# Optimization experiments

Hardware: AMD Instinct MI355X
Metric: run time of the kernel (lower is better)

The kernel has to match this reference:

```python
import jax, jax.numpy as jnp
import numpy as np

DIM = 768
HEADS = 12
MLP_DIM = 3072
EPS = 1e-5


def setup_inputs() -> dict:
    key = jax.random.key(0)
    ks = jax.random.split(key, 10)
    s = lambda d: 1.0 / np.sqrt(d)
    return {
        "x": jax.random.normal(ks[0], (8, 1024, DIM), dtype=jnp.float32),
        "ln1_g": jnp.ones((DIM,), jnp.float32),
        "ln1_b": jnp.zeros((DIM,), jnp.float32),
        "w_qkv": jax.random.normal(ks[1], (DIM, 3 * DIM), jnp.float32) * s(DIM),
        "w_out": jax.random.normal(ks[2], (DIM, DIM), jnp.float32) * s(DIM),
        "b_out": jnp.zeros((DIM,), jnp.float32),
        "ln2_g": jnp.ones((DIM,), jnp.float32),
        "ln2_b": jnp.zeros((DIM,), jnp.float32),
        "w1": jax.random.normal(ks[3], (DIM, MLP_DIM), jnp.float32) * s(DIM),
        "b1": jnp.zeros((MLP_DIM,), jnp.float32),
        "w2": jax.random.normal(ks[4], (MLP_DIM, DIM), jnp.float32) * s(MLP_DIM),
        "b2": jnp.zeros((DIM,), jnp.float32),
    }


def _layernorm(x, g, b):
    mu = jnp.mean(x, axis=-1, keepdims=True)
    var = jnp.mean(jnp.square(x - mu), axis=-1, keepdims=True)
    return (x - mu) * jax.lax.rsqrt(var + EPS) * g + b


def _block(x, ln1_g, ln1_b, w_qkv, w_out, b_out, ln2_g, ln2_b, w1, b1, w2, b2):
    B, N, C = x.shape
    H = HEADS
    Dh = C // H
    scale = Dh ** -0.5
    # attention
    h = _layernorm(x, ln1_g, ln1_b)
    qkv = (h @ w_qkv).reshape(B, N, 3, H, Dh)
    q, k, v = qkv[:, :, 0], qkv[:, :, 1], qkv[:, :, 2]  # [B,N,H,Dh]
    attn = jnp.einsum("bnhd,bmhd->bhnm", q, k) * scale
    attn = jax.nn.softmax(attn, axis=-1)
    o = jnp.einsum("bhnm,bmhd->bnhd", attn, v).reshape(B, N, C)
    x = x + o @ w_out + b_out
    # mlp (exact erf GELU, matching torch nn.GELU default)
    h = _layernorm(x, ln2_g, ln2_b)
    h = jax.nn.gelu(h @ w1 + b1, approximate=False)
    x = x + h @ w2 + b2
    return x


def reference(x, ln1_g, ln1_b, w_qkv, w_out, b_out, ln2_g, ln2_b, w1, b1, w2, b2):
    return _block(x, ln1_g, ln1_b, w_qkv, w_out, b_out, ln2_g, ln2_b, w1, b1, w2, b2)
```

## Files before the change

kernel.cpp:

```cpp
#include <hip/hip_runtime.h>
#include <hip/hip_bf16.h>
#include <cstdint>

#define DIM 768
#define HEADS 12
#define DH 64
#define MLP_DIM 3072
#define ROWS 8192
#define SEQ 1024
#define PPAD 72
#define ISTR 136
#define FSTR 132

typedef __attribute__((ext_vector_type(8))) short bf16x8;
typedef __attribute__((ext_vector_type(4))) float f32x4;

typedef __attribute__((address_space(1))) void GV;
typedef __attribute__((address_space(3))) void SV;

__device__ inline void async16(const void* g, void* l) {
  __builtin_amdgcn_global_load_lds((GV*)(void*)g, (SV*)l, 16, 0, 0);
}

__device__ inline unsigned short f2b(float f) {
  union { float f; uint32_t u; } v; v.f = f;
  uint32_t u = v.u;
  return (unsigned short)((u + 0x7fffu + ((u >> 16) & 1u)) >> 16);
}

__device__ inline float gelu_f(float v) {
  float x = v * 0.70710678118654752f;
  float ax = fabsf(x);
  float t = 1.f / (1.f + 0.47047f * ax);
  float poly = t * (0.3480242f + t * (-0.0958798f + t * 0.7478556f));
  float erfv = 1.f - poly * __expf(-ax * ax);
  erfv = copysignf(erfv, x);
  return 0.5f * v * (1.f + erfv);
}

__global__ __launch_bounds__(256) void transpose_k(const float* __restrict__ in,
                                                   unsigned short* __restrict__ out,
                                                   int K, int N) {
  __shared__ float t[32][33];
  int tx = threadIdx.x & 31, ty = threadIdx.x >> 5;
  int bn = blockIdx.x * 32, bk = blockIdx.y * 32;
#pragma unroll
  for (int i = ty; i < 32; i += 8) t[i][tx] = in[(size_t)(bk + i) * N + bn + tx];
  __syncthreads();
#pragma unroll
  for (int i = ty; i < 32; i += 8) out[(size_t)(bn + i) * K + bk + tx] = f2b(t[tx][i]);
}

__global__ __launch_bounds__(256) void ln_k(const float* __restrict__ x,
                                            const float* __restrict__ g,
                                            const float* __restrict__ b,
                                            unsigned short* __restrict__ h) {
  int wave = threadIdx.x >> 6, lane = threadIdx.x & 63;
  int row = blockIdx.x * 4 + wave;
  const float* xr = x + (size_t)row * DIM;
  float v[12];
  float s = 0.f;
#pragma unroll
  for (int j = 0; j < 12; ++j) { v[j] = xr[lane + j * 64]; s += v[j]; }
#pragma unroll
  for (int m = 1; m < 64; m <<= 1) s += __shfl_xor(s, m);
  float mu = s * (1.f / DIM);
  float vs = 0.f;
#pragma unroll
  for (int j = 0; j < 12; ++j) { float d = v[j] - mu; vs += d * d; }
#pragma unroll
  for (int m = 1; m < 64; m <<= 1) vs += __shfl_xor(vs, m);
  float rstd = rsqrtf(vs * (1.f / DIM) + 1e-5f);
  unsigned short* hr = h + (size_t)row * DIM;
#pragma unroll
  for (int j = 0; j < 12; ++j) {
    int i = lane + j * 64;
    hr[i] = f2b((v[j] - mu) * rstd * g[i] + b[i]);
  }
}

template <int MODE, int TM>
__global__ __launch_bounds__(256, 2) void gemm_k(
    const unsigned short* __restrict__ A, const unsigned short* __restrict__ Bt,
    int M, int N, int K,
    const float* __restrict__ bias, const float* __restrict__ resid,
    float* __restrict__ outf, unsigned short* __restrict__ outb,
    unsigned short* __restrict__ Qb, unsigned short* __restrict__ Kb,
    unsigned short* __restrict__ Vt) {
  constexpr int MI = (TM == 128) ? 4 : 2;
  constexpr int ASZ = TM * 64, BSZ = 128 * 64;
  __shared__ __align__(16) unsigned short smem[2 * (ASZ + BSZ)];
  int tid = threadIdx.x;
  int wave = tid >> 6, lane = tid & 63, lrow = lane & 15, qd = lane >> 4;
  int ntn = N >> 7;
  int bm = (blockIdx.x / ntn) * TM;
  int bn = (blockIdx.x % ntn) << 7;
  int wm = (TM == 128) ? (wave >> 1) * 64 : (wave & 1) * 32;
  int wn = (TM == 128) ? (wave & 1) * 64 : (wave >> 1) * 64;

  f32x4 acc[MI][4];
#pragma unroll
  for (int i = 0; i < MI; ++i)
#pragma unroll
    for (int j = 0; j < 4; ++j) acc[i][j] = (f32x4){0.f, 0.f, 0.f, 0.f};

  int srow = tid >> 3;
  int c = (tid & 7) ^ (srow & 7);
  const char* gA = (const char*)(A + (size_t)(bm + srow) * K) + c * 16;
  const char* gB = (const char*)(Bt + (size_t)(bn + srow) * K) + c * 16;
  size_t rstep = (size_t)32 * K * 2;

  auto stage = [&](int kt, int buf) {
    size_t ko = (size_t)kt * 128;
    char* lA = (char*)(smem + (size_t)buf * (ASZ + BSZ)) + tid * 16;
    char* lB = lA + ASZ * 2;
#pragma unroll
    for (int j = 0; j < TM / 32; ++j) async16(gA + ko + j * rstep, lA + j * 4096);
#pragma unroll
    for (int j = 0; j < 4; ++j) async16(gB + ko + j * rstep, lB + j * 4096);
  };

  int nk = K >> 6;
  stage(0, 0);
  for (int kt = 0; kt < nk; ++kt) {
    asm volatile("s_waitcnt vmcnt(0)" ::: "memory");
    __syncthreads();
    if (kt + 1 < nk) stage(kt + 1, (kt + 1) & 1);
    const unsigned short* As = smem + (size_t)(kt & 1) * (ASZ + BSZ);
    const unsigned short* Bs = As + ASZ;
#pragma unroll
    for (int s = 0; s < 2; ++s) {
      int q = s * 4 + qd;
      bf16x8 af[MI], bfr[4];
#pragma unroll
      for (int i = 0; i < MI; ++i) {
        int r = wm + i * 16 + lrow;
        af[i] = *(const bf16x8*)(As + r * 64 + ((q ^ (r & 7)) << 3));
      }
#pragma unroll
      for (int i = 0; i < 4; ++i) {
        int r = wn + i * 16 + lrow;
        bfr[i] = *(const bf16x8*)(Bs + r * 64 + ((q ^ (r & 7)) << 3));
      }
#pragma unroll
      for (int mi = 0; mi < MI; ++mi)
#pragma unroll
        for (int ni = 0; ni < 4; ++ni)
          acc[mi][ni] = __builtin_amdgcn_mfma_f32_16x16x32_bf16(af[mi], bfr[ni], acc[mi][ni], 0, 0, 0);
    }
  }
  __syncthreads();

  if (MODE == 1) {
    float* img = (float*)smem;
#pragma unroll
    for (int mi = 0; mi < MI; ++mi)
#pragma unroll
      for (int ni = 0; ni < 4; ++ni)
#pragma unroll
        for (int r = 0; r < 4; ++r)
          img[(wm + mi * 16 + qd * 4 + r) * FSTR + wn + ni * 16 + lrow] = acc[mi][ni][r];
    __syncthreads();
    int lr = tid >> 2, cs = (tid & 3) * 32;
    const float* src = img + lr * FSTR + cs;
    float* dst = outf + (size_t)(bm + lr) * 768 + bn + cs;
    const float* bp = bias + bn + cs;
    const float* rp = resid + (size_t)(bm + lr) * 768 + bn + cs;
#pragma unroll
    for (int k = 0; k < 8; ++k) {
      f32x4 v = *(const f32x4*)(src + k * 4);
      f32x4 bb = *(const f32x4*)(bp + k * 4);
      f32x4 rr = *(const f32x4*)(rp + k * 4);
      *(f32x4*)(dst + k * 4) = v + bb + rr;
    }
  } else if (MODE == 2) {
    unsigned short* img = smem;
#pragma unroll
    for (int mi = 0; mi < MI; ++mi)
#pragma unroll
      for (int ni = 0; ni < 4; ++ni)
#pragma unroll
        for (int r = 0; r < 4; ++r) {
          int lc = wn + ni * 16 + lrow;
          float v = acc[mi][ni][r] + bias[bn + lc];
          img[(wm + mi * 16 + qd * 4 + r) * ISTR + lc] = f2b(gelu_f(v));
        }
    __syncthreads();
#pragma unroll
    for (int p = 0; p < 2; ++p) {
      int lr = p * 64 + (tid >> 2);
      int cs = (tid & 3) * 32;
      const unsigned short* src = img + lr * ISTR + cs;
      unsigned short* dst = outb + (size_t)(bm + lr) * MLP_DIM + bn + cs;
#pragma unroll
      for (int k = 0; k < 4; ++k) *(uint4*)(dst + k * 8) = *(const uint4*)(src + k * 8);
    }
  } else {
    int which = bn / 768;
    int rem_base = bn - which * 768;
    unsigned short* img = smem;
    if (which < 2) {
#pragma unroll
      for (int mi = 0; mi < MI; ++mi)
#pragma unroll
        for (int ni = 0; ni < 4; ++ni)
#pragma unroll
          for (int r = 0; r < 4; ++r) {
            float v = acc[mi][ni][r];
            if (which == 0) v *= 0.125f;
            img[(wm + mi * 16 + qd * 4 + r) * ISTR + wn + ni * 16 + lrow] = f2b(v);
          }
      __syncthreads();
      int lr = tid >> 1, hseg = tid & 1;
      int hh = rem_base / 64 + hseg;
      int b = (bm + lr) >> 10, n = (bm + lr) & 1023;
      size_t bh = (size_t)(b * HEADS + hh);
      const unsigned short* src = img + lr * ISTR + hseg * 64;
      unsigned short* dst = (which == 0 ? Qb : Kb) + (bh * SEQ + n) * DH;
      if (which == 0) {
#pragma unroll
        for (int j = 0; j < 8; ++j) *(uint4*)(dst + j * 8) = *(const uint4*)(src + j * 8);
      } else {
        int nx = n & 7;
#pragma unroll
        for (int j = 0; j < 8; ++j) *(uint4*)(dst + ((j ^ nx) * 8)) = *(const uint4*)(src + j * 8);
      }
    } else {
#pragma unroll
      for (int mi = 0; mi < MI; ++mi)
#pragma unroll
        for (int ni = 0; ni < 4; ++ni) {
          int lc = wn + ni * 16 + lrow;
          int rbase = wm + mi * 16 + qd * 4;
          uint2 pk;
          pk.x = (uint32_t)f2b(acc[mi][ni][0]) | ((uint32_t)f2b(acc[mi][ni][1]) << 16);
          pk.y = (uint32_t)f2b(acc[mi][ni][2]) | ((uint32_t)f2b(acc[mi][ni][3]) << 16);
          *(uint2*)(img + lc * ISTR + rbase) = pk;
        }
      __syncthreads();
      int d = tid >> 1, nh = tid & 1;
      int hh = rem_base / 64 + (d >> 6);
      int dhl = d & 63;
      int b = bm >> 10;
      size_t bh = (size_t)(b * HEADS + hh);
      const unsigned short* src = img + d * ISTR + nh * 64;
      unsigned short* dst = Vt + (bh * DH + dhl) * SEQ + (bm & 1023) + nh * 64;
      int dx = dhl & 7;
#pragma unroll
      for (int j = 0; j < 8; ++j) *(uint4*)(dst + ((j ^ dx) * 8)) = *(const uint4*)(src + j * 8);
    }
  }
}

__global__ __launch_bounds__(256, 3) void attn_k(const unsigned short* __restrict__ Qb,
                                                 const unsigned short* __restrict__ Kb,
                                                 const unsigned short* __restrict__ Vt,
                                                 unsigned short* __restrict__ o) {
  __shared__ __align__(16) unsigned short Ks[2][64 * 64];
  __shared__ __align__(16) unsigned short Vs[2][64 * 64];
  __shared__ __align__(16) unsigned short Pa[4][32 * PPAD];
  int tid = threadIdx.x;
  int wave = tid >> 6, lane = tid & 63;
  int lrow = lane & 15, qd = lane >> 4;
  int bh = blockIdx.x % 96;
  int qt = blockIdx.x / 96;
  int b = bh / HEADS, hh = bh % HEADS;
  const unsigned short* Qh = Qb + (size_t)bh * SEQ * DH;
  const char* Kh = (const char*)(Kb + (size_t)bh * SEQ * DH);
  const char* Vh = (const char*)(Vt + (size_t)bh * DH * SEQ);
  int qw = qt * 128 + wave * 32;

  bf16x8 qf[2][2];
#pragma unroll
  for (int qs = 0; qs < 2; ++qs)
#pragma unroll
    for (int hf = 0; hf < 2; ++hf)
      qf[qs][hf] = *(const bf16x8*)(Qh + (qw + qs * 16 + lrow) * DH + hf * 32 + qd * 8);

  f32x4 oacc[2][4];
#pragma unroll
  for (int qs = 0; qs < 2; ++qs)
#pragma unroll
    for (int d = 0; d < 4; ++d) oacc[qs][d] = (f32x4){0.f, 0.f, 0.f, 0.f};
  float li[2] = {0.f, 0.f};
  unsigned short* Pw = Pa[wave];

  auto stage = [&](int t, int buf) {
    const char* kbase = Kh + (size_t)t * 8192;
    char* kd = (char*)Ks[buf];
    async16(kbase + tid * 16, kd + tid * 16);
    async16(kbase + 4096 + tid * 16, kd + 4096 + tid * 16);
    const char* vbase = Vh + (size_t)t * 128;
    char* vd = (char*)Vs[buf];
    async16(vbase + (size_t)(tid >> 3) * 2048 + (tid & 7) * 16, vd + tid * 16);
    async16(vbase + (size_t)((tid >> 3) + 32) * 2048 + (tid & 7) * 16, vd + 4096 + tid * 16);
  };

  stage(0, 0);
  for (int t = 0; t < 16; ++t) {
    asm volatile("s_waitcnt vmcnt(0)" ::: "memory");
    __syncthreads();
    if (t < 15) stage(t + 1, (t + 1) & 1);
    const unsigned short* Kst = Ks[t & 1];
    const unsigned short* Vst = Vs[t & 1];

    f32x4 st[4][2];
#pragma unroll
    for (int kt = 0; kt < 4; ++kt) {
      int krow = kt * 16 + lrow;
      int ksw = krow & 7;
      const unsigned short* Kr = Kst + krow * 64;
      bf16x8 k0 = *(const bf16x8*)(Kr + ((qd ^ ksw) << 3));
      bf16x8 k1 = *(const bf16x8*)(Kr + (((qd + 4) ^ ksw) << 3));
#pragma unroll
      for (int qs = 0; qs < 2; ++qs) {
        f32x4 z = (f32x4){0.f, 0.f, 0.f, 0.f};
        z = __builtin_amdgcn_mfma_f32_16x16x32_bf16(k0, qf[qs][0], z, 0, 0, 0);
        z = __builtin_amdgcn_mfma_f32_16x16x32_bf16(k1, qf[qs][1], z, 0, 0, 0);
        st[kt][qs] = z;
      }
    }

#pragma unroll
    for (int kt = 0; kt < 4; ++kt)
#pragma unroll
      for (int qs = 0; qs < 2; ++qs) {
        float p0 = __expf(st[kt][qs][0]);
        float p1 = __expf(st[kt][qs][1]);
        float p2 = __expf(st[kt][qs][2]);
        float p3 = __expf(st[kt][qs][3]);
        li[qs] += (p0 + p1) + (p2 + p3);
        uint2 pk;
        pk.x = (uint32_t)f2b(p0) | ((uint32_t)f2b(p1) << 16);
        pk.y = (uint32_t)f2b(p2) | ((uint32_t)f2b(p3) << 16);
        *(uint2*)(Pw + (qs * 16 + lrow) * PPAD + kt * 16 + qd * 4) = pk;
      }
    asm volatile("s_waitcnt lgkmcnt(0)" ::: "memory");

    bf16x8 ap[2][2];
#pragma unroll
    for (int qs = 0; qs < 2; ++qs)
#pragma unroll
      for (int kh = 0; kh < 2; ++kh)
        ap[qs][kh] = *(const bf16x8*)(Pw + (qs * 16 + lrow) * PPAD + kh * 32 + qd * 8);

#pragma unroll
    for (int ds = 0; ds < 4; ++ds) {
      int vrow = ds * 16 + lrow;
      int vsw = vrow & 7;
      const unsigned short* Vr = Vst + vrow * 64;
      bf16x8 v0 = *(const bf16x8*)(Vr + ((qd ^ vsw) << 3));
      bf16x8 v1 = *(const bf16x8*)(Vr + (((4 + qd) ^ vsw) << 3));
#pragma unroll
      for (int qs = 0; qs < 2; ++qs) {
        oacc[qs][ds] = __builtin_amdgcn_mfma_f32_16x16x32_bf16(ap[qs][0], v0, oacc[qs][ds], 0, 0, 0);
        oacc[qs][ds] = __builtin_amdgcn_mfma_f32_16x16x32_bf16(ap[qs][1], v1, oacc[qs][ds], 0, 0, 0);
      }
    }
  }

#pragma unroll
  for (int qs = 0; qs < 2; ++qs) {
    li[qs] += __shfl_xor(li[qs], 16);
    li[qs] += __shfl_xor(li[qs], 32);
  }

#pragma unroll
  for (int qs = 0; qs < 2; ++qs)
#pragma unroll
    for (int r = 0; r < 4; ++r) {
      float inv = 1.f / __shfl(li[qs], qd * 4 + r);
      int n = qw + qs * 16 + qd * 4 + r;
#pragma unroll
      for (int ds = 0; ds < 4; ++ds) {
        int dh = ds * 16 + lrow;
        o[((size_t)(b * SEQ + n)) * DIM + hh * DH + dh] = f2b(oacc[qs][ds][r] * inv);
      }
    }
}

extern "C" void kernel_launch(void* const* d_in, const int* in_sizes, int n_in,
                              void* d_out, int out_size, void* d_ws, size_t ws_size,
                              hipStream_t stream) {
  const float* x     = (const float*)d_in[0];
  const float* ln1_g = (const float*)d_in[1];
  const float* ln1_b = (const float*)d_in[2];
  const float* w_qkv = (const float*)d_in[3];
  const float* w_out = (const float*)d_in[4];
  const float* b_out = (const float*)d_in[5];
  const float* ln2_g = (const float*)d_in[6];
  const float* ln2_b = (const float*)d_in[7];
  const float* w1    = (const float*)d_in[8];
  const float* b1    = (const float*)d_in[9];
  const float* w2    = (const float*)d_in[10];
  const float* b2    = (const float*)d_in[11];

  char* ws = (char*)d_ws;
  unsigned short* wqkvT = (unsigned short*)(ws + 0);
  unsigned short* woutT = (unsigned short*)(ws + 3538944);
  unsigned short* w1T   = (unsigned short*)(ws + 4718592);
  unsigned short* w2T   = (unsigned short*)(ws + 9437184);
  float*          x2    = (float*)(ws + 14155776);
  unsigned short* h     = (unsigned short*)(ws + 39321600);
  char* big = ws + 51904512;
  unsigned short* Qb = (unsigned short*)(big);
  unsigned short* Kb = (unsigned short*)(big + 12582912);
  unsigned short* Vt = (unsigned short*)(big + 25165824);
  unsigned short* ob = (unsigned short*)(big + 37748736);
  unsigned short* am = (unsigned short*)(big);

  transpose_k<<<dim3(72, 24), 256, 0, stream>>>(w_qkv, wqkvT, 768, 2304);
  transpose_k<<<dim3(24, 24), 256, 0, stream>>>(w_out, woutT, 768, 768);
  transpose_k<<<dim3(96, 24), 256, 0, stream>>>(w1, w1T, 768, 3072);
  transpose_k<<<dim3(24, 96), 256, 0, stream>>>(w2, w2T, 3072, 768);

  ln_k<<<2048, 256, 0, stream>>>(x, ln1_g, ln1_b, h);
  gemm_k<0, 128><<<64 * 18, 256, 0, stream>>>(h, wqkvT, ROWS, 2304, 768,
                                              nullptr, nullptr, nullptr, nullptr, Qb, Kb, Vt);
  attn_k<<<768, 256, 0, stream>>>(Qb, Kb, Vt, ob);
  gemm_k<1, 64><<<128 * 6, 256, 0, stream>>>(ob, woutT, ROWS, 768, 768,
                                             b_out, x, x2, nullptr, nullptr, nullptr, nullptr);
  ln_k<<<2048, 256, 0, stream>>>(x2, ln2_g, ln2_b, h);
  gemm_k<2, 128><<<64 * 24, 256, 0, stream>>>(h, w1T, ROWS, 3072, 768,
                                              b1, nullptr, nullptr, am, nullptr, nullptr, nullptr);
  gemm_k<1, 64><<<128 * 6, 256, 0, stream>>>(am, w2T, ROWS, 768, 3072,
                                             b2, x2, (float*)d_out, nullptr, nullptr, nullptr, nullptr);
}
```

Measured before the change: 391.4 us.

## Split GEMM into single-buffered variants with larger per-wave tiles

Replaces the templated double-buffered GEMM with two kernels. QKV and MLP-up use 128 threads, each wave computing a 64x128 tile, which raises register-level reuse. Output projections use a single-buffered 64x128 tile and write the bias and residual epilogue directly from registers instead of staging through LDS. Dropping double buffering serializes loads and MFMA within each block and leaves overlap to other resident blocks. The larger accumulators also raise register pressure and may lower occupancy.

```diff
diff --git a/kernel.cpp b/kernel.cpp
--- a/kernel.cpp
+++ b/kernel.cpp
@@ -10,7 +10,6 @@
 #define SEQ 1024
 #define PPAD 72
 #define ISTR 136
-#define FSTR 132
 
 typedef __attribute__((ext_vector_type(8))) short bf16x8;
 typedef __attribute__((ext_vector_type(4))) float f32x4;
@@ -79,28 +78,24 @@
   }
 }
 
-template <int MODE, int TM>
-__global__ __launch_bounds__(256, 2) void gemm_k(
+__global__ __launch_bounds__(256, 2) void gemm1_k(
     const unsigned short* __restrict__ A, const unsigned short* __restrict__ Bt,
-    int M, int N, int K,
+    int N, int K,
     const float* __restrict__ bias, const float* __restrict__ resid,
-    float* __restrict__ outf, unsigned short* __restrict__ outb,
-    unsigned short* __restrict__ Qb, unsigned short* __restrict__ Kb,
-    unsigned short* __restrict__ Vt) {
-  constexpr int MI = (TM == 128) ? 4 : 2;
-  constexpr int ASZ = TM * 64, BSZ = 128 * 64;
-  __shared__ __align__(16) unsigned short smem[2 * (ASZ + BSZ)];
+    float* __restrict__ outf) {
+  __shared__ __align__(16) unsigned short As[64 * 64];
+  __shared__ __align__(16) unsigned short Bs[128 * 64];
   int tid = threadIdx.x;
   int wave = tid >> 6, lane = tid & 63, lrow = lane & 15, qd = lane >> 4;
   int ntn = N >> 7;
-  int bm = (blockIdx.x / ntn) * TM;
+  int bm = (blockIdx.x / ntn) * 64;
   int bn = (blockIdx.x % ntn) << 7;
-  int wm = (TM == 128) ? (wave >> 1) * 64 : (wave & 1) * 32;
-  int wn = (TM == 128) ? (wave & 1) * 64 : (wave >> 1) * 64;
-
-  f32x4 acc[MI][4];
-#pragma unroll
-  for (int i = 0; i < MI; ++i)
+  int wm = (wave & 1) * 32;
+  int wn = (wave >> 1) * 64;
+
+  f32x4 acc[2][4];
+#pragma unroll
+  for (int i = 0; i < 2; ++i)
 #pragma unroll
     for (int j = 0; j < 4; ++j) acc[i][j] = (f32x4){0.f, 0.f, 0.f, 0.f};
 
@@ -108,32 +103,25 @@
   int c = (tid & 7) ^ (srow & 7);
   const char* gA = (const char*)(A + (size_t)(bm + srow) * K) + c * 16;
   const char* gB = (const char*)(Bt + (size_t)(bn + srow) * K) + c * 16;
+  char* lA = (char*)As + tid * 16;
+  char* lB = (char*)Bs + tid * 16;
   size_t rstep = (size_t)32 * K * 2;
 
-  auto stage = [&](int kt, int buf) {
+  int nk = K >> 6;
+  for (int kt = 0; kt < nk; ++kt) {
     size_t ko = (size_t)kt * 128;
-    char* lA = (char*)(smem + (size_t)buf * (ASZ + BSZ)) + tid * 16;
-    char* lB = lA + ASZ * 2;
-#pragma unroll
-    for (int j = 0; j < TM / 32; ++j) async16(gA + ko + j * rstep, lA + j * 4096);
+#pragma unroll
+    for (int j = 0; j < 2; ++j) async16(gA + ko + j * rstep, lA + j * 4096);
 #pragma unroll
     for (int j = 0; j < 4; ++j) async16(gB + ko + j * rstep, lB + j * 4096);
-  };
-
-  int nk = K >> 6;
-  stage(0, 0);
-  for (int kt = 0; kt < nk; ++kt) {
     asm volatile("s_waitcnt vmcnt(0)" ::: "memory");
     __syncthreads();
-    if (kt + 1 < nk) stage(kt + 1, (kt + 1) & 1);
-    const unsigned short* As = smem + (size_t)(kt & 1) * (ASZ + BSZ);
-    const unsigned short* Bs = As + ASZ;
 #pragma unroll
     for (int s = 0; s < 2; ++s) {
       int q = s * 4 + qd;
-      bf16x8 af[MI], bfr[4];
-#pragma unroll
-      for (int i = 0; i < MI; ++i) {
+      bf16x8 af[2], bfr[4];
+#pragma unroll
+      for (int i = 0; i < 2; ++i) {
         int r = wm + i * 16 + lrow;
         af[i] = *(const bf16x8*)(As + r * 64 + ((q ^ (r & 7)) << 3));
       }
@@ -143,52 +131,107 @@
         bfr[i] = *(const bf16x8*)(Bs + r * 64 + ((q ^ (r & 7)) << 3));
       }
 #pragma unroll
-      for (int mi = 0; mi < MI; ++mi)
+      for (int mi = 0; mi < 2; ++mi)
 #pragma unroll
         for (int ni = 0; ni < 4; ++ni)
           acc[mi][ni] = __builtin_amdgcn_mfma_f32_16x16x32_bf16(af[mi], bfr[ni], acc[mi][ni], 0, 0, 0);
     }
-  }
-  __syncthreads();
-
-  if (MODE == 1) {
-    float* img = (float*)smem;
-#pragma unroll
-    for (int mi = 0; mi < MI; ++mi)
-#pragma unroll
-      for (int ni = 0; ni < 4; ++ni)
-#pragma unroll
-        for (int r = 0; r < 4; ++r)
-          img[(wm + mi * 16 + qd * 4 + r) * FSTR + wn + ni * 16 + lrow] = acc[mi][ni][r];
-    __syncthreads();
-    int lr = tid >> 2, cs = (tid & 3) * 32;
-    const float* src = img + lr * FSTR + cs;
-    float* dst = outf + (size_t)(bm + lr) * 768 + bn + cs;
-    const float* bp = bias + bn + cs;
-    const float* rp = resid + (size_t)(bm + lr) * 768 + bn + cs;
-#pragma unroll
-    for (int k = 0; k < 8; ++k) {
-      f32x4 v = *(const f32x4*)(src + k * 4);
-      f32x4 bb = *(const f32x4*)(bp + k * 4);
-      f32x4 rr = *(const f32x4*)(rp + k * 4);
-      *(f32x4*)(dst + k * 4) = v + bb + rr;
-    }
-  } else if (MODE == 2) {
-    unsigned short* img = smem;
-#pragma unroll
-    for (int mi = 0; mi < MI; ++mi)
-#pragma unroll
-      for (int ni = 0; ni < 4; ++ni)
+    __syncthreads();
+  }
+
+#pragma unroll
+  for (int mi = 0; mi < 2; ++mi)
+#pragma unroll
+    for (int ni = 0; ni < 4; ++ni)
+#pragma unroll
+      for (int r = 0; r < 4; ++r) {
+        int row = bm + wm + mi * 16 + qd * 4 + r;
+        int col = bn + wn + ni * 16 + lrow;
+        float v = acc[mi][ni][r] + bias[col] + resid[(size_t)row * 768 + col];
+        outf[(size_t)row * 768 + col] = v;
+      }
+}
+
+template <int MODE>
+__global__ __launch_bounds__(128, 2) void gemm2_k(
+    const unsigned short* __restrict__ A, const unsigned short* __restrict__ Bt,
+    int N, int K,
+    const float* __restrict__ bias, unsigned short* __restrict__ outb,
+    unsigned short* __restrict__ Qb, unsigned short* __restrict__ Kb,
+    unsigned short* __restrict__ Vt) {
+  __shared__ __align__(16) unsigned short smem[128 * ISTR];
+  int tid = threadIdx.x;
+  int wave = tid >> 6, lane = tid & 63, lrow = lane & 15, qd = lane >> 4;
+  int ntn = N >> 7;
+  int bm = (blockIdx.x / ntn) << 7;
+  int bn = (blockIdx.x % ntn) << 7;
+  int wm = wave * 64;
+
+  f32x4 acc[4][8];
+#pragma unroll
+  for (int i = 0; i < 4; ++i)
+#pragma unroll
+    for (int j = 0; j < 8; ++j) acc[i][j] = (f32x4){0.f, 0.f, 0.f, 0.f};
+
+  int srow = tid >> 3;
+  int c = (tid & 7) ^ (srow & 7);
+  const char* gA = (const char*)(A + (size_t)(bm + srow) * K) + c * 16;
+  const char* gB = (const char*)(Bt + (size_t)(bn + srow) * K) + c * 16;
+  char* lA = (char*)smem + tid * 16;
+  char* lB = (char*)smem + 16384 + tid * 16;
+  size_t rstep = (size_t)16 * K * 2;
+
+  const unsigned short* As = smem;
+  const unsigned short* Bs = smem + 8192;
+
+  int nk = K >> 6;
+  for (int kt = 0; kt < nk; ++kt) {
+    size_t ko = (size_t)kt * 128;
+#pragma unroll
+    for (int j = 0; j < 8; ++j) async16(gA + ko + j * rstep, lA + j * 2048);
+#pragma unroll
+    for (int j = 0; j < 8; ++j) async16(gB + ko + j * rstep, lB + j * 2048);
+    asm volatile("s_waitcnt vmcnt(0)" ::: "memory");
+    __syncthreads();
+#pragma unroll
+    for (int s = 0; s < 2; ++s) {
+      int q = s * 4 + qd;
+      bf16x8 af[4], bfr[8];
+#pragma unroll
+      for (int i = 0; i < 4; ++i) {
+        int r = wm + i * 16 + lrow;
+        af[i] = *(const bf16x8*)(As + r * 64 + ((q ^ (r & 7)) << 3));
+      }
+#pragma unroll
+      for (int i = 0; i < 8; ++i) {
+        int r = i * 16 + lrow;
+        bfr[i] = *(const bf16x8*)(Bs + r * 64 + ((q ^ (r & 7)) << 3));
+      }
+#pragma unroll
+      for (int mi = 0; mi < 4; ++mi)
+#pragma unroll
+        for (int ni = 0; ni < 8; ++ni)
+          acc[mi][ni] = __builtin_amdgcn_mfma_f32_16x16x32_bf16(af[mi], bfr[ni], acc[mi][ni], 0, 0, 0);
+    }
+    __syncthreads();
+  }
+
+  unsigned short* img = smem;
+  if (MODE == 2) {
+#pragma unroll
+    for (int mi = 0; mi < 4; ++mi)
+#pragma unroll
+      for (int ni = 0; ni < 8; ++ni)
 #pragma unroll
         for (int r = 0; r < 4; ++r) {
-          int lc = wn + ni * 16 + lrow;
+          int lc = ni * 16 + lrow;
           float v = acc[mi][ni][r] + bias[bn + lc];
           img[(wm + mi * 16 + qd * 4 + r) * ISTR + lc] = f2b(gelu_f(v));
         }
     __syncthreads();
 #pragma unroll
-    for (int p = 0; p < 2; ++p) {
-      int lr = p * 64 + (tid >> 2);
+    for (int p = 0; p < 4; ++p) {
+      int lr = p * 32 + (tid >> 2);
       int cs = (tid & 3) * 32;
       const unsigned short* src = img + lr * ISTR + cs;
       unsigned short* dst = outb + (size_t)(bm + lr) * MLP_DIM + bn + cs;
@@ -198,39 +241,41 @@
   } else {
     int which = bn / 768;
     int rem_base = bn - which * 768;
-    unsigned short* img = smem;
     if (which < 2) {
 #pragma unroll
-      for (int mi = 0; mi < MI; ++mi)
-#pragma unroll
-        for (int ni = 0; ni < 4; ++ni)
+      for (int mi = 0; mi < 4; ++mi)
+#pragma unroll
+        for (int ni = 0; ni < 8; ++ni)
 #pragma unroll
           for (int r = 0; r < 4; ++r) {
             float v = acc[mi][ni][r];
             if (which == 0) v *= 0.125f;
-            img[(wm + mi * 16 + qd * 4 + r) * ISTR + wn + ni * 16 + lrow] = f2b(v);
+            img[(wm + mi * 16 + qd * 4 + r) * ISTR + ni * 16 + lrow] = f2b(v);
           }
       __syncthreads();
-      int lr = tid >> 1, hseg = tid & 1;
-      int hh = rem_base / 64 + hseg;
+      int lr = tid;
       int b = (bm + lr) >> 10, n = (bm + lr) & 1023;
-      size_t bh = (size_t)(b * HEADS + hh);
-      const unsigned short* src = img + lr * ISTR + hseg * 64;
-      unsigned short* dst = (which == 0 ? Qb : Kb) + (bh * SEQ + n) * DH;
-      if (which == 0) {
-#pragma unroll
-        for (int j = 0; j < 8; ++j) *(uint4*)(dst + j * 8) = *(const uint4*)(src + j * 8);
-      } else {
-        int nx = n & 7;
-#pragma unroll
-        for (int j = 0; j < 8; ++j) *(uint4*)(dst + ((j ^ nx) * 8)) = *(const uint4*)(src + j * 8);
+#pragma unroll
+      for (int hseg = 0; hseg < 2; ++hseg) {
+        int hh = rem_base / 64 + hseg;
+        size_t bh = (size_t)(b * HEADS + hh);
+        const unsigned short* src = img + lr * ISTR + hseg * 64;
+        unsigned short* dst = (which == 0 ? Qb : Kb) + (bh * SEQ + n) * DH;
+        if (which == 0) {
+#pragma unroll
+          for (int j = 0; j < 8; ++j) *(uint4*)(dst + j * 8) = *(const uint4*)(src + j * 8);
+        } else {
+          int nx = n & 7;
+#pragma unroll
+          for (int j = 0; j < 8; ++j) *(uint4*)(dst + ((j ^ nx) * 8)) = *(const uint4*)(src + j * 8);
+        }
       }
     } else {
 #pragma unroll
-      for (int mi = 0; mi < MI; ++mi)
-#pragma unroll
-        for (int ni = 0; ni < 4; ++ni) {
-          int lc = wn + ni * 16 + lrow;
+      for (int mi = 0; mi < 4; ++mi)
+#pragma unroll
+        for (int ni = 0; ni < 8; ++ni) {
+          int lc = ni * 16 + lrow;
           int rbase = wm + mi * 16 + qd * 4;
           uint2 pk;
           pk.x = (uint32_t)f2b(acc[mi][ni][0]) | ((uint32_t)f2b(acc[mi][ni][1]) << 16);
@@ -238,16 +283,20 @@
           *(uint2*)(img + lc * ISTR + rbase) = pk;
         }
       __syncthreads();
-      int d = tid >> 1, nh = tid & 1;
+      int d = tid;
       int hh = rem_base / 64 + (d >> 6);
       int dhl = d & 63;
       int b = bm >> 10;
       size_t bh = (size_t)(b * HEADS + hh);
-      const unsigned short* src = img + d * ISTR + nh * 64;
-      unsigned short* dst = Vt + (bh * DH + dhl) * SEQ + (bm & 1023) + nh * 64;
+      const unsigned short* src = img + d * ISTR;
       int dx = dhl & 7;
 #pragma unroll
-      for (int j = 0; j < 8; ++j) *(uint4*)(dst + ((j ^ dx) * 8)) = *(const uint4*)(src + j * 8);
+      for (int nh = 0; nh < 2; ++nh) {
+        unsigned short* dst = Vt + (bh * DH + dhl) * SEQ + (bm & 1023) + nh * 64;
+#pragma unroll
+        for (int j = 0; j < 8; ++j)
+          *(uint4*)(dst + ((j ^ dx) * 8)) = *(const uint4*)(src + nh * 64 + j * 8);
+      }
     }
   }
 }
@@ -415,14 +464,12 @@
   transpose_k<<<dim3(24, 96), 256, 0, stream>>>(w2, w2T, 3072, 768);
 
   ln_k<<<2048, 256, 0, stream>>>(x, ln1_g, ln1_b, h);
-  gemm_k<0, 128><<<64 * 18, 256, 0, stream>>>(h, wqkvT, ROWS, 2304, 768,
-                                              nullptr, nullptr, nullptr, nullptr, Qb, Kb, Vt);
+  gemm2_k<0><<<64 * 18, 128, 0, stream>>>(h, wqkvT, 2304, 768,
+                                          nullptr, nullptr, Qb, Kb, Vt);
   attn_k<<<768, 256, 0, stream>>>(Qb, Kb, Vt, ob);
-  gemm_k<1, 64><<<128 * 6, 256, 0, stream>>>(ob, woutT, ROWS, 768, 768,
-                                             b_out, x, x2, nullptr, nullptr, nullptr, nullptr);
+  gemm1_k<<<128 * 6, 256, 0, stream>>>(ob, woutT, 768, 768, b_out, x, x2);
   ln_k<<<2048, 256, 0, stream>>>(x2, ln2_g, ln2_b, h);
-  gemm_k<2, 128><<<64 * 24, 256, 0, stream>>>(h, w1T, ROWS, 3072, 768,
-                                              b1, nullptr, nullptr, am, nullptr, nullptr, nullptr);
-  gemm_k<1, 64><<<128 * 6, 256, 0, stream>>>(am, w2T, ROWS, 768, 3072,
-                                             b2, x2, (float*)d_out, nullptr, nullptr, nullptr, nullptr);
-}
+  gemm2_k<2><<<64 * 24, 128, 0, stream>>>(h, w1T, 3072, 768,
+                                          b1, am, nullptr, nullptr, nullptr);
+  gemm1_k<<<128 * 6, 256, 0, stream>>>(am, w2T, 768, 3072, b2, x2, (float*)d_out);
+}
```

New measurement: 374.0 us. 1.05x faster.

## Replace async double-buffered LDS GEMM with register-prefetch single buffer

Applied to the files above, without the earlier changes.

The GEMM mainloop no longer uses global_load_lds into two LDS buffers. It now prefetches the next K-tile into registers, stores it into a single LDS buffer and adds a second barrier per iteration. The MODE 1 epilogue drops its LDS staging and writes bias plus residual directly from the accumulators with scalar, uncoalesced accesses. This halves LDS use, which may raise occupancy, but it costs extra VGPRs, an extra sync per k-step and poorer store coalescing.

```diff
diff --git a/kernel.cpp b/kernel.cpp
--- a/kernel.cpp
+++ b/kernel.cpp
@@ -10,7 +10,6 @@
 #define SEQ 1024
 #define PPAD 72
 #define ISTR 136
-#define FSTR 132
 
 typedef __attribute__((ext_vector_type(8))) short bf16x8;
 typedef __attribute__((ext_vector_type(4))) float f32x4;
@@ -82,14 +81,15 @@
 template <int MODE, int TM>
 __global__ __launch_bounds__(256, 2) void gemm_k(
     const unsigned short* __restrict__ A, const unsigned short* __restrict__ Bt,
-    int M, int N, int K,
+    int N, int K,
     const float* __restrict__ bias, const float* __restrict__ resid,
     float* __restrict__ outf, unsigned short* __restrict__ outb,
     unsigned short* __restrict__ Qb, unsigned short* __restrict__ Kb,
     unsigned short* __restrict__ Vt) {
   constexpr int MI = (TM == 128) ? 4 : 2;
-  constexpr int ASZ = TM * 64, BSZ = 128 * 64;
-  __shared__ __align__(16) unsigned short smem[2 * (ASZ + BSZ)];
+  constexpr int ASH = TM * 64;
+  constexpr int SMEMS = (TM == 128) ? 128 * ISTR : (ASH + 8192);
+  __shared__ __align__(16) unsigned short smem[SMEMS];
   int tid = threadIdx.x;
   int wave = tid >> 6, lane = tid & 63, lrow = lane & 15, qd = lane >> 4;
   int ntn = N >> 7;
@@ -108,26 +108,31 @@
   int c = (tid & 7) ^ (srow & 7);
   const char* gA = (const char*)(A + (size_t)(bm + srow) * K) + c * 16;
   const char* gB = (const char*)(Bt + (size_t)(bn + srow) * K) + c * 16;
+  char* lA = (char*)smem + tid * 16;
+  char* lB = (char*)smem + ASH * 2 + tid * 16;
   size_t rstep = (size_t)32 * K * 2;
 
-  auto stage = [&](int kt, int buf) {
+  const unsigned short* As = smem;
+  const unsigned short* Bs = smem + ASH;
+
+  uint4 pa[TM / 32], pb[4];
+  auto loadt = [&](int kt) {
     size_t ko = (size_t)kt * 128;
-    char* lA = (char*)(smem + (size_t)buf * (ASZ + BSZ)) + tid * 16;
-    char* lB = lA + ASZ * 2;
-#pragma unroll
-    for (int j = 0; j < TM / 32; ++j) async16(gA + ko + j * rstep, lA + j * 4096);
-#pragma unroll
-    for (int j = 0; j < 4; ++j) async16(gB + ko + j * rstep, lB + j * 4096);
+#pragma unroll
+    for (int j = 0; j < TM / 32; ++j) pa[j] = *(const uint4*)(gA + ko + j * rstep);
+#pragma unroll
+    for (int j = 0; j < 4; ++j) pb[j] = *(const uint4*)(gB + ko + j * rstep);
   };
 
   int nk = K >> 6;
-  stage(0, 0);
+  loadt(0);
   for (int kt = 0; kt < nk; ++kt) {
-    asm volatile("s_waitcnt vmcnt(0)" ::: "memory");
+#pragma unroll
+    for (int j = 0; j < TM / 32; ++j) *(uint4*)(lA + j * 4096) = pa[j];
+#pragma unroll
+    for (int j = 0; j < 4; ++j) *(uint4*)(lB + j * 4096) = pb[j];
     __syncthreads();
-    if (kt + 1 < nk) stage(kt + 1, (kt + 1) & 1);
-    const unsigned short* As = smem + (size_t)(kt & 1) * (ASZ + BSZ);
-    const unsigned short* Bs = As + ASZ;
+    if (kt + 1 < nk) loadt(kt + 1);
 #pragma unroll
     for (int s = 0; s < 2; ++s) {
       int q = s * 4 + qd;
@@ -148,31 +153,21 @@
         for (int ni = 0; ni < 4; ++ni)
           acc[mi][ni] = __builtin_amdgcn_mfma_f32_16x16x32_bf16(af[mi], bfr[ni], acc[mi][ni], 0, 0, 0);
     }
+    __syncthreads();
   }
-  __syncthreads();
 
   if (MODE == 1) {
-    float* img = (float*)smem;
 #pragma unroll
     for (int mi = 0; mi < MI; ++mi)
 #pragma unroll
       for (int ni = 0; ni < 4; ++ni)
 #pragma unroll
-        for (int r = 0; r < 4; ++r)
-          img[(wm + mi * 16 + qd * 4 + r) * FSTR + wn + ni * 16 + lrow] = acc[mi][ni][r];
-    __syncthreads();
-    int lr = tid >> 2, cs = (tid & 3) * 32;
-    const float* src = img + lr * FSTR + cs;
-    float* dst = outf + (size_t)(bm + lr) * 768 + bn + cs;
-    const float* bp = bias + bn + cs;
-    const float* rp = resid + (size_t)(bm + lr) * 768 + bn + cs;
-#pragma unroll
-    for (int k = 0; k < 8; ++k) {
-      f32x4 v = *(const f32x4*)(src + k * 4);
-      f32x4 bb = *(const f32x4*)(bp + k * 4);
-      f32x4 rr = *(const f32x4*)(rp + k * 4);
-      *(f32x4*)(dst + k * 4) = v + bb + rr;
-    }
+        for (int r = 0; r < 4; ++r) {
+          int row = bm + wm + mi * 16 + qd * 4 + r;
+          int col = bn + wn + ni * 16 + lrow;
+          float v = acc[mi][ni][r] + bias[col] + resid[(size_t)row * 768 + col];
+          outf[(size_t)row * 768 + col] = v;
+        }
   } else if (MODE == 2) {
     unsigned short* img = smem;
 #pragma unroll
@@ -415,14 +410,14 @@
   transpose_k<<<dim3(24, 96), 256, 0, stream>>>(w2, w2T, 3072, 768);
 
   ln_k<<<2048, 256, 0, stream>>>(x, ln1_g, ln1_b, h);
-  gemm_k<0, 128><<<64 * 18, 256, 0, stream>>>(h, wqkvT, ROWS, 2304, 768,
+  gemm_k<0, 128><<<64 * 18, 256, 0, stream>>>(h, wqkvT, 2304, 768,
                                               nullptr, nullptr, nullptr, nullptr, Qb, Kb, Vt);
   attn_k<<<768, 256, 0, stream>>>(Qb, Kb, Vt, ob);
-  gemm_k<1, 64><<<128 * 6, 256, 0, stream>>>(ob, woutT, ROWS, 768, 768,
+  gemm_k<1, 64><<<128 * 6, 256, 0, stream>>>(ob, woutT, 768, 768,
                                              b_out, x, x2, nullptr, nullptr, nullptr, nullptr);
   ln_k<<<2048, 256, 0, stream>>>(x2, ln2_g, ln2_b, h);
-  gemm_k<2, 128><<<64 * 24, 256, 0, stream>>>(h, w1T, ROWS, 3072, 768,
+  gemm_k<2, 128><<<64 * 24, 256, 0, stream>>>(h, w1T, 3072, 768,
                                               b1, nullptr, nullptr, am, nullptr, nullptr, nullptr);
-  gemm_k<1, 64><<<128 * 6, 256, 0, stream>>>(am, w2T, ROWS, 768, 3072,
+  gemm_k<1, 64><<<128 * 6, 256, 0, stream>>>(am, w2T, 768, 3072,
                                              b2, x2, (float*)d_out, nullptr, nullptr, nullptr, nullptr);
 }
```

Result: slower. 896.4 us (+129.0%).
